# Kernel optimization log

Measured on AMD Instinct MI355X. Metric: run time of the kernel, lower is better.

## Reference

```python
import jax, jax.numpy as jnp
import numpy as np

M, K, N = 8192, 4096, 4096  # tokens, in_features, out_features

def setup_inputs() -> dict:
    key = jax.random.key(0)
    k1, k2, k3 = jax.random.split(key, 3)
    x = jax.random.normal(k1, (M, K), dtype=jnp.float32)
    # kaiming_uniform_(a=sqrt(5)) on [out,in] -> uniform(-1/sqrt(in), 1/sqrt(in))
    bound = 1.0 / np.sqrt(K)
    weight = jax.random.uniform(k2, (N, K), dtype=jnp.float32, minval=-bound, maxval=bound)
    bias = jax.random.uniform(k3, (N,), dtype=jnp.float32, minval=-bound, maxval=bound)
    return {
        "x": x,
        "weight": weight,
        "bias": bias,
        "input_scale": jnp.float32(1.0),
        "weight_scale": jnp.float32(1.0),
    }


def reference(x, weight, bias, input_scale, weight_scale):
    # Quantize input and weight to fp8 e4m3 (per-tensor scale = 1.0 in module),
    # then dequant-matmul: out = (x_fp8 @ w_fp8^T) * scale_a * scale_b + bias,
    # matching torch._scaled_mm semantics with out_dtype=float32.
    x_fp8 = x.astype(jnp.float8_e4m3fn)
    w_fp8 = weight.astype(jnp.float8_e4m3fn)
    out = jnp.einsum(
        "mk,nk->mn",
        x_fp8.astype(jnp.float32),
        w_fp8.astype(jnp.float32),
    ) * (input_scale * weight_scale)
    return out + bias[None, :]
```

## Files before the change

kernel.cpp:

```cpp
#include <hip/hip_runtime.h>
#include <hip/hip_fp8.h>
#include <cstdint>

typedef float f32x4 __attribute__((ext_vector_type(4)));
typedef int i32x8 __attribute__((ext_vector_type(8)));
typedef long long i64;

static constexpr int Mdim = 8192;
static constexpr int Kdim = 4096;
static constexpr int Ndim = 4096;
static constexpr int BM = 128, BN = 128, BK = 128;
static constexpr int NWG_M = Mdim / BM;
static constexpr int NWG_N = Ndim / BN;
static constexpr int NWG = NWG_M * NWG_N;

__device__ __forceinline__ uint8_t f32_to_e4m3(float f) {
  return (uint8_t)__hip_cvt_float_to_fp8(f, __HIP_SATFINITE, __HIP_E4M3);
}

__global__ __launch_bounds__(256) void quant_fp8_kernel(
    const float* __restrict__ in, uint8_t* __restrict__ out, int n_vec16) {
  const int stride = gridDim.x * blockDim.x;
  for (int i = blockIdx.x * blockDim.x + threadIdx.x; i < n_vec16; i += stride) {
    const float4* src = reinterpret_cast<const float4*>(in) + (size_t)i * 4;
    float4 f0 = src[0], f1 = src[1], f2 = src[2], f3 = src[3];
    const float v[16] = {f0.x, f0.y, f0.z, f0.w, f1.x, f1.y, f1.z, f1.w,
                         f2.x, f2.y, f2.z, f2.w, f3.x, f3.y, f3.z, f3.w};
    union alignas(16) {
      uint32_t u[4];
      uint8_t b[16];
    } r;
#pragma unroll
    for (int j = 0; j < 16; ++j) r.b[j] = f32_to_e4m3(v[j]);
    reinterpret_cast<uint4*>(out)[i] = *reinterpret_cast<const uint4*>(r.u);
  }
}

__device__ __forceinline__ void gload_lds16(const uint8_t* g, uint8_t* l) {
  __builtin_amdgcn_global_load_lds(
      (const __attribute__((address_space(1))) void*)g,
      (__attribute__((address_space(3))) void*)l, 16, 0, 0);
}

__global__ __launch_bounds__(256) void gemm_fp8_mx_kernel(
    const uint8_t* __restrict__ Aq, const uint8_t* __restrict__ Bq,
    const float* __restrict__ bias, const float* __restrict__ sa,
    const float* __restrict__ sb, float* __restrict__ C) {
  __shared__ alignas(16) uint8_t As[BM * BK];
  __shared__ alignas(16) uint8_t Bs[BN * BK];

  int wg = (int)blockIdx.x;
  wg = (wg & 7) * (NWG / 8) + (wg >> 3);
  const int bm0 = (wg / NWG_N) * BM;
  const int bn0 = (wg % NWG_N) * BN;

  const int t = (int)threadIdx.x;
  const int lane = t & 63;
  const int wave = t >> 6;
  const int wm = wave >> 1, wn = wave & 1;

  const int srow = t >> 3;
  const int sc16 = (t & 7) ^ (srow & 7);
  const uint8_t* aSrc[4];
  const uint8_t* bSrc[4];
#pragma unroll
  for (int i = 0; i < 4; ++i) {
    const int row = i * 32 + srow;
    aSrc[i] = Aq + (size_t)(bm0 + row) * Kdim + sc16 * 16;
    bSrc[i] = Bq + (size_t)(bn0 + row) * Kdim + sc16 * 16;
  }

  const int r7 = lane & 7;
  const int kg = (lane >> 4) * 2;
  const int off0 = ((kg ^ r7) * 16);
  const int off1 = (((kg + 1) ^ r7) * 16);
  const int rbA = (wm * 64 + (lane & 15)) * BK;
  const int rbB = (wn * 64 + (lane & 15)) * BK;

  f32x4 acc[4][4] = {};

  for (int kt = 0; kt < Kdim / BK; ++kt) {
    const int kb = kt * BK;
#pragma unroll
    for (int i = 0; i < 4; ++i) {
      gload_lds16(aSrc[i] + kb, As + (i * 256 + t) * 16);
      gload_lds16(bSrc[i] + kb, Bs + (i * 256 + t) * 16);
    }
    __syncthreads();

    i32x8 af[4], bf[4];
#pragma unroll
    for (int m = 0; m < 4; ++m) {
      const int rb = rbA + m * 16 * BK;
      union {
        i32x8 v;
        int4 h[2];
      } u;
      u.h[0] = *reinterpret_cast<const int4*>(As + rb + off0);
      u.h[1] = *reinterpret_cast<const int4*>(As + rb + off1);
      af[m] = u.v;
    }
#pragma unroll
    for (int n = 0; n < 4; ++n) {
      const int rb = rbB + n * 16 * BK;
      union {
        i32x8 v;
        int4 h[2];
      } u;
      u.h[0] = *reinterpret_cast<const int4*>(Bs + rb + off0);
      u.h[1] = *reinterpret_cast<const int4*>(Bs + rb + off1);
      bf[n] = u.v;
    }

#pragma unroll
    for (int m = 0; m < 4; ++m)
#pragma unroll
      for (int n = 0; n < 4; ++n)
        acc[m][n] = __builtin_amdgcn_mfma_scale_f32_16x16x128_f8f6f4(
            af[m], bf[n], acc[m][n],  0,  0,
             0, 0x7f7f7f7f,  0, 0x7f7f7f7f);
    __syncthreads();
  }

  const float scale = sa[0] * sb[0];
  const int orow0 = bm0 + wm * 64 + ((lane >> 4) << 2);
  const int ocol0 = bn0 + wn * 64 + (lane & 15);
#pragma unroll
  for (int n = 0; n < 4; ++n) {
    const int col = ocol0 + n * 16;
    const float bv = bias[col];
#pragma unroll
    for (int m = 0; m < 4; ++m) {
      const int row = orow0 + m * 16;
#pragma unroll
      for (int r = 0; r < 4; ++r)
        C[(size_t)(row + r) * Ndim + col] = acc[m][n][r] * scale + bv;
    }
  }
}

__device__ __forceinline__ void stage16_cvt(const float* g, uint8_t* l) {
  const float4* s = reinterpret_cast<const float4*>(g);
  float4 f0 = s[0], f1 = s[1], f2 = s[2], f3 = s[3];
  const float v[16] = {f0.x, f0.y, f0.z, f0.w, f1.x, f1.y, f1.z, f1.w,
                       f2.x, f2.y, f2.z, f2.w, f3.x, f3.y, f3.z, f3.w};
  union alignas(16) {
    uint32_t u[4];
    uint8_t b[16];
  } r;
#pragma unroll
  for (int j = 0; j < 16; ++j) r.b[j] = f32_to_e4m3(v[j]);
  *reinterpret_cast<uint4*>(l) = *reinterpret_cast<const uint4*>(r.u);
}

__global__ __launch_bounds__(256) void gemm_fp8_fused_kernel(
    const float* __restrict__ X, const float* __restrict__ W,
    const float* __restrict__ bias, const float* __restrict__ sa,
    const float* __restrict__ sb, float* __restrict__ C) {
  constexpr int FBK = 64;
  __shared__ alignas(16) uint8_t As[BM * FBK];
  __shared__ alignas(16) uint8_t Bs[BN * FBK];

  int wg = (int)blockIdx.x;
  wg = (wg & 7) * (NWG / 8) + (wg >> 3);
  const int bm0 = (wg / NWG_N) * BM;
  const int bn0 = (wg % NWG_N) * BN;

  const int t = (int)threadIdx.x;
  const int lane = t & 63;
  const int wave = t >> 6;
  const int wm = wave >> 1, wn = wave & 1;

  const int c0 = t, c1 = t + 256;
  const int r0 = c0 >> 2, col0 = (c0 & 3) * 16;
  const int r1 = c1 >> 2, col1 = (c1 & 3) * 16;
  const float* xa0 = X + (size_t)(bm0 + r0) * Kdim + col0;
  const float* xa1 = X + (size_t)(bm0 + r1) * Kdim + col1;
  const float* wb0 = W + (size_t)(bn0 + r0) * Kdim + col0;
  const float* wb1 = W + (size_t)(bn0 + r1) * Kdim + col1;

  const int arow = (wm * 64 + (lane & 15)) * FBK;
  const int brow = (wn * 64 + (lane & 15)) * FBK;
  const int koff = (lane >> 4) * 8;

  f32x4 acc[4][4] = {};

  for (int kt = 0; kt < Kdim / FBK; ++kt) {
    const int kb = kt * FBK;
    stage16_cvt(xa0 + kb, As + c0 * 16);
    stage16_cvt(xa1 + kb, As + c1 * 16);
    stage16_cvt(wb0 + kb, Bs + c0 * 16);
    stage16_cvt(wb1 + kb, Bs + c1 * 16);
    __syncthreads();
#pragma unroll
    for (int kk = 0; kk < FBK / 32; ++kk) {
      i64 a[4], b[4];
#pragma unroll
      for (int m = 0; m < 4; ++m)
        a[m] = *reinterpret_cast<const i64*>(&As[arow + m * 16 * FBK + kk * 32 + koff]);
#pragma unroll
      for (int n = 0; n < 4; ++n)
        b[n] = *reinterpret_cast<const i64*>(&Bs[brow + n * 16 * FBK + kk * 32 + koff]);
#pragma unroll
      for (int m = 0; m < 4; ++m)
#pragma unroll
        for (int n = 0; n < 4; ++n)
          acc[m][n] = __builtin_amdgcn_mfma_f32_16x16x32_fp8_fp8(
              a[m], b[n], acc[m][n], 0, 0, 0);
    }
    __syncthreads();
  }

  const float scale = sa[0] * sb[0];
  const int orow0 = bm0 + wm * 64 + ((lane >> 4) << 2);
  const int ocol0 = bn0 + wn * 64 + (lane & 15);
#pragma unroll
  for (int n = 0; n < 4; ++n) {
    const int col = ocol0 + n * 16;
    const float bv = bias[col];
#pragma unroll
    for (int m = 0; m < 4; ++m) {
      const int row = orow0 + m * 16;
#pragma unroll
      for (int r = 0; r < 4; ++r)
        C[(size_t)(row + r) * Ndim + col] = acc[m][n][r] * scale + bv;
    }
  }
}

extern "C" void kernel_launch(void* const* d_in, const int* in_sizes, int n_in,
                              void* d_out, int out_size, void* d_ws, size_t ws_size,
                              hipStream_t stream) {
  const float* x = (const float*)d_in[0];
  const float* w = (const float*)d_in[1];
  const float* bias = (const float*)d_in[2];
  const float* s_in = (const float*)d_in[3];
  const float* s_w = (const float*)d_in[4];
  float* out = (float*)d_out;

  const size_t needA = (size_t)Mdim * Kdim;
  const size_t needB = (size_t)Ndim * Kdim;

  if (ws_size >= needA + needB) {
    uint8_t* Aq = (uint8_t*)d_ws;
    uint8_t* Bq = Aq + needA;
    quant_fp8_kernel<<<2048, 256, 0, stream>>>(x, Aq, (int)(needA / 16));
    quant_fp8_kernel<<<2048, 256, 0, stream>>>(w, Bq, (int)(needB / 16));
    gemm_fp8_mx_kernel<<<NWG, 256, 0, stream>>>(Aq, Bq, bias, s_in, s_w, out);
  } else {
    gemm_fp8_fused_kernel<<<NWG, 256, 0, stream>>>(x, w, bias, s_in, s_w, out);
  }
}
```

Measured before the change: 204.6 us.

## Use 256x256 tiles with double-buffered LDS and 512-thread pipelined MX GEMM

```diff
diff --git a/kernel.cpp b/kernel.cpp
--- a/kernel.cpp
+++ b/kernel.cpp
@@ -9,10 +9,13 @@
 static constexpr int Mdim = 8192;
 static constexpr int Kdim = 4096;
 static constexpr int Ndim = 4096;
-static constexpr int BM = 128, BN = 128, BK = 128;
+
+static constexpr int BM = 256, BN = 256, BK = 128;
+static constexpr int NT = Kdim / BK;
 static constexpr int NWG_M = Mdim / BM;
 static constexpr int NWG_N = Ndim / BN;
 static constexpr int NWG = NWG_M * NWG_N;
+static_assert(NT >= 4, "pipeline needs >=4 K-tiles");
 
 __device__ __forceinline__ uint8_t f32_to_e4m3(float f) {
   return (uint8_t)__hip_cvt_float_to_fp8(f, __HIP_SATFINITE, __HIP_E4M3);
@@ -42,12 +45,17 @@
       (__attribute__((address_space(3))) void*)l, 16, 0, 0);
 }
 
-__global__ __launch_bounds__(256) void gemm_fp8_mx_kernel(
+__device__ __forceinline__ f32x4 mx_mfma(i32x8 a, i32x8 b, f32x4 c) {
+  return __builtin_amdgcn_mfma_scale_f32_16x16x128_f8f6f4(
+      a, b, c, 0, 0, 0, 0x7f7f7f7f, 0, 0x7f7f7f7f);
+}
+
+__global__ __launch_bounds__(512, 2) void gemm_fp8_mx_256(
     const uint8_t* __restrict__ Aq, const uint8_t* __restrict__ Bq,
     const float* __restrict__ bias, const float* __restrict__ sa,
     const float* __restrict__ sb, float* __restrict__ C) {
-  __shared__ alignas(16) uint8_t As[BM * BK];
-  __shared__ alignas(16) uint8_t Bs[BN * BK];
+  __shared__ alignas(16) uint8_t sA[2][BM * BK];
+  __shared__ alignas(16) uint8_t sB[2][BN * BK];
 
   int wg = (int)blockIdx.x;
   wg = (wg & 7) * (NWG / 8) + (wg >> 3);
@@ -57,80 +65,121 @@
   const int t = (int)threadIdx.x;
   const int lane = t & 63;
   const int wave = t >> 6;
-  const int wm = wave >> 1, wn = wave & 1;
+  const int wm = wave >> 2;
+  const int wn = wave & 3;
 
   const int srow = t >> 3;
   const int sc16 = (t & 7) ^ (srow & 7);
-  const uint8_t* aSrc[4];
-  const uint8_t* bSrc[4];
-#pragma unroll
-  for (int i = 0; i < 4; ++i) {
-    const int row = i * 32 + srow;
-    aSrc[i] = Aq + (size_t)(bm0 + row) * Kdim + sc16 * 16;
-    bSrc[i] = Bq + (size_t)(bn0 + row) * Kdim + sc16 * 16;
-  }
+  const uint8_t* aBase = Aq + (size_t)(bm0 + srow) * Kdim + sc16 * 16;
+  const uint8_t* bBase = Bq + (size_t)(bn0 + srow) * Kdim + sc16 * 16;
+  const int ldsOff = t * 16;
+
+  auto stage = [&](int buf, int kt) {
+    const int kb = kt * BK;
+#pragma unroll
+    for (int i = 0; i < 4; ++i)
+      gload_lds16(aBase + kb + (size_t)i * (64 * Kdim),
+                  &sA[buf][i * 8192 + ldsOff]);
+#pragma unroll
+    for (int i = 0; i < 4; ++i)
+      gload_lds16(bBase + kb + (size_t)i * (64 * Kdim),
+                  &sB[buf][i * 8192 + ldsOff]);
+  };
 
   const int r7 = lane & 7;
   const int kg = (lane >> 4) * 2;
-  const int off0 = ((kg ^ r7) * 16);
-  const int off1 = (((kg + 1) ^ r7) * 16);
-  const int rbA = (wm * 64 + (lane & 15)) * BK;
+  const int off0 = (kg ^ r7) * 16;
+  const int off1 = ((kg + 1) ^ r7) * 16;
+  const int rbA = (wm * 128 + (lane & 15)) * BK;
   const int rbB = (wn * 64 + (lane & 15)) * BK;
 
-  f32x4 acc[4][4] = {};
-
-  for (int kt = 0; kt < Kdim / BK; ++kt) {
-    const int kb = kt * BK;
-#pragma unroll
-    for (int i = 0; i < 4; ++i) {
-      gload_lds16(aSrc[i] + kb, As + (i * 256 + t) * 16);
-      gload_lds16(bSrc[i] + kb, Bs + (i * 256 + t) * 16);
+  auto ldfrag = [&](const uint8_t* base) -> i32x8 {
+    union {
+      i32x8 v;
+      int4 h[2];
+    } u;
+    u.h[0] = *reinterpret_cast<const int4*>(base + off0);
+    u.h[1] = *reinterpret_cast<const int4*>(base + off1);
+    return u.v;
+  };
+
+  f32x4 acc[8][4] = {};
+
+  stage(0, 0);
+  stage(1, 1);
+  asm volatile("s_waitcnt vmcnt(8)" ::: "memory");
+  __builtin_amdgcn_s_barrier();
+  asm volatile("" ::: "memory");
+
+#pragma unroll 1
+  for (int kt = 0; kt < NT; ++kt) {
+    const int c = kt & 1;
+    const uint8_t* A = &sA[c][0];
+    const uint8_t* B = &sB[c][0];
+
+    i32x8 bf[4];
+#pragma unroll
+    for (int n = 0; n < 4; ++n) bf[n] = ldfrag(B + rbB + n * 16 * BK);
+    i32x8 a0 = ldfrag(A + rbA + 0 * 16 * BK);
+    i32x8 a1 = ldfrag(A + rbA + 1 * 16 * BK);
+    __builtin_amdgcn_s_setprio(1);
+#pragma unroll
+    for (int n = 0; n < 4; ++n) acc[0][n] = mx_mfma(a0, bf[n], acc[0][n]);
+#pragma unroll
+    for (int n = 0; n < 4; ++n) acc[1][n] = mx_mfma(a1, bf[n], acc[1][n]);
+    __builtin_amdgcn_s_setprio(0);
+
+    a0 = ldfrag(A + rbA + 2 * 16 * BK);
+    a1 = ldfrag(A + rbA + 3 * 16 * BK);
+    __builtin_amdgcn_s_setprio(1);
+#pragma unroll
+    for (int n = 0; n < 4; ++n) acc[2][n] = mx_mfma(a0, bf[n], acc[2][n]);
+#pragma unroll
+    for (int n = 0; n < 4; ++n) acc[3][n] = mx_mfma(a1, bf[n], acc[3][n]);
+    __builtin_amdgcn_s_setprio(0);
+
+    a0 = ldfrag(A + rbA + 4 * 16 * BK);
+    a1 = ldfrag(A + rbA + 5 * 16 * BK);
+    __builtin_amdgcn_s_setprio(1);
+#pragma unroll
+    for (int n = 0; n < 4; ++n) acc[4][n] = mx_mfma(a0, bf[n], acc[4][n]);
+#pragma unroll
+    for (int n = 0; n < 4; ++n) acc[5][n] = mx_mfma(a1, bf[n], acc[5][n]);
+    __builtin_amdgcn_s_setprio(0);
+
+    a0 = ldfrag(A + rbA + 6 * 16 * BK);
+    a1 = ldfrag(A + rbA + 7 * 16 * BK);
+    asm volatile("s_waitcnt lgkmcnt(0)" ::: "memory");
+    __builtin_amdgcn_s_barrier();
+    asm volatile("" ::: "memory");
+    if (kt + 2 < NT) stage(c, kt + 2);
+    __builtin_amdgcn_s_setprio(1);
+#pragma unroll
+    for (int n = 0; n < 4; ++n) acc[6][n] = mx_mfma(a0, bf[n], acc[6][n]);
+#pragma unroll
+    for (int n = 0; n < 4; ++n) acc[7][n] = mx_mfma(a1, bf[n], acc[7][n]);
+    __builtin_amdgcn_s_setprio(0);
+
+    if (kt + 2 < NT) {
+      asm volatile("s_waitcnt vmcnt(8)" ::: "memory");
+      __builtin_amdgcn_s_barrier();
+      asm volatile("" ::: "memory");
+    } else if (kt + 1 < NT) {
+      asm volatile("s_waitcnt vmcnt(0)" ::: "memory");
+      __builtin_amdgcn_s_barrier();
+      asm volatile("" ::: "memory");
     }
-    __syncthreads();
-
-    i32x8 af[4], bf[4];
-#pragma unroll
-    for (int m = 0; m < 4; ++m) {
-      const int rb = rbA + m * 16 * BK;
-      union {
-        i32x8 v;
-        int4 h[2];
-      } u;
-      u.h[0] = *reinterpret_cast<const int4*>(As + rb + off0);
-      u.h[1] = *reinterpret_cast<const int4*>(As + rb + off1);
-      af[m] = u.v;
-    }
-#pragma unroll
-    for (int n = 0; n < 4; ++n) {
-      const int rb = rbB + n * 16 * BK;
-      union {
-        i32x8 v;
-        int4 h[2];
-      } u;
-      u.h[0] = *reinterpret_cast<const int4*>(Bs + rb + off0);
-      u.h[1] = *reinterpret_cast<const int4*>(Bs + rb + off1);
-      bf[n] = u.v;
-    }
-
-#pragma unroll
-    for (int m = 0; m < 4; ++m)
-#pragma unroll
-      for (int n = 0; n < 4; ++n)
-        acc[m][n] = __builtin_amdgcn_mfma_scale_f32_16x16x128_f8f6f4(
-            af[m], bf[n], acc[m][n],  0,  0,
-             0, 0x7f7f7f7f,  0, 0x7f7f7f7f);
-    __syncthreads();
   }
 
   const float scale = sa[0] * sb[0];
-  const int orow0 = bm0 + wm * 64 + ((lane >> 4) << 2);
+  const int orow0 = bm0 + wm * 128 + ((lane >> 4) << 2);
   const int ocol0 = bn0 + wn * 64 + (lane & 15);
 #pragma unroll
   for (int n = 0; n < 4; ++n) {
     const int col = ocol0 + n * 16;
     const float bv = bias[col];
 #pragma unroll
-    for (int m = 0; m < 4; ++m) {
+    for (int m = 0; m < 8; ++m) {
       const int row = orow0 + m * 16;
 #pragma unroll
       for (int r = 0; r < 4; ++r)
@@ -157,14 +206,16 @@
     const float* __restrict__ X, const float* __restrict__ W,
     const float* __restrict__ bias, const float* __restrict__ sa,
     const float* __restrict__ sb, float* __restrict__ C) {
-  constexpr int FBK = 64;
-  __shared__ alignas(16) uint8_t As[BM * FBK];
-  __shared__ alignas(16) uint8_t Bs[BN * FBK];
+  constexpr int FBM = 128, FBN = 128, FBK = 64;
+  constexpr int FNWG_N = Ndim / FBN;
+  __shared__ alignas(16) uint8_t As[FBM * FBK];
+  __shared__ alignas(16) uint8_t Bs[FBN * FBK];
 
   int wg = (int)blockIdx.x;
-  wg = (wg & 7) * (NWG / 8) + (wg >> 3);
-  const int bm0 = (wg / NWG_N) * BM;
-  const int bn0 = (wg % NWG_N) * BN;
+  const int nwg = (Mdim / FBM) * FNWG_N;
+  wg = (wg & 7) * (nwg / 8) + (wg >> 3);
+  const int bm0 = (wg / FNWG_N) * FBM;
+  const int bn0 = (wg % FNWG_N) * FBN;
 
   const int t = (int)threadIdx.x;
   const int lane = t & 63;
@@ -246,8 +297,9 @@
     uint8_t* Bq = Aq + needA;
     quant_fp8_kernel<<<2048, 256, 0, stream>>>(x, Aq, (int)(needA / 16));
     quant_fp8_kernel<<<2048, 256, 0, stream>>>(w, Bq, (int)(needB / 16));
-    gemm_fp8_mx_kernel<<<NWG, 256, 0, stream>>>(Aq, Bq, bias, s_in, s_w, out);
+    gemm_fp8_mx_256<<<NWG, 512, 0, stream>>>(Aq, Bq, bias, s_in, s_w, out);
   } else {
-    gemm_fp8_fused_kernel<<<NWG, 256, 0, stream>>>(x, w, bias, s_in, s_w, out);
-  }
-}
+    gemm_fp8_fused_kernel<<<(Mdim / 128) * (Ndim / 128), 256, 0, stream>>>(
+        x, w, bias, s_in, s_w, out);
+  }
+}
```

Result: faster. 196.9 us (-3.8%).
